# Kernel optimization log

Measured on AMD Instinct MI355X. Metric: run time of the kernel, lower is better.

Reference implementation:

```python
import jax, jax.numpy as jnp
import numpy as np
from jax import lax

V, E, H, K = 100000, 256, 512, 12
B, T = 64, 256
START, END, PAD = 10, 11, 0
NEG = -100000.0


def setup_inputs() -> dict:
    key = jax.random.key(0)
    ks = jax.random.split(key, 16)
    Hd = H // 2
    def n(k, shape, s=0.1):
        return jax.random.normal(k, shape, jnp.float32) * s
    sentence = jax.random.randint(ks[0], (B, T), 0, V)
    sentence_chars = jnp.zeros((B, T, 16), jnp.int32)
    emb = jax.random.normal(ks[1], (V, E), jnp.float32)
    Wih_f, Whh_f = n(ks[2], (4 * Hd, E)), n(ks[3], (4 * Hd, Hd))
    bih_f, bhh_f = n(ks[4], (4 * Hd,)), n(ks[5], (4 * Hd,))
    Wih_b, Whh_b = n(ks[6], (4 * Hd, E)), n(ks[7], (4 * Hd, Hd))
    bih_b, bhh_b = n(ks[8], (4 * Hd,)), n(ks[9], (4 * Hd,))
    Wp, bp = n(ks[10], (K, H)), n(ks[11], (K,))
    # transitions[i, j] = score of transitioning from tag j to tag i
    trans = jax.random.normal(ks[12], (K, K), jnp.float32)
    trans = trans.at[START, :].set(NEG)
    trans = trans.at[:, END].set(NEG)
    trans = trans.at[:, PAD].set(NEG)
    trans = trans.at[PAD, :].set(NEG)
    trans = trans.at[PAD, PAD].set(0.0)
    trans = trans.at[PAD, END].set(0.0)
    h0 = jax.random.normal(ks[13], (2, B, Hd), jnp.float32)
    c0 = jax.random.normal(ks[14], (2, B, Hd), jnp.float32)
    return dict(sentence=sentence, sentence_chars=sentence_chars, emb=emb,
                Wih_f=Wih_f, Whh_f=Whh_f, bih_f=bih_f, bhh_f=bhh_f,
                Wih_b=Wih_b, Whh_b=Whh_b, bih_b=bih_b, bhh_b=bhh_b,
                Wp=Wp, bp=bp, transitions=trans, h0=h0, c0=c0)


def _lstm_dir(x, Wih, Whh, bih, bhh, h, c, reverse):
    # x: [B, T, E] -> hs: [B, T, Hd]; PyTorch LSTM gate order i,f,g,o
    def step(carry, xt):
        h, c = carry
        g = xt @ Wih.T + bih + h @ Whh.T + bhh
        i, f, gg, o = jnp.split(g, 4, axis=-1)
        c = jax.nn.sigmoid(f) * c + jax.nn.sigmoid(i) * jnp.tanh(gg)
        h = jax.nn.sigmoid(o) * jnp.tanh(c)
        return (h, c), h
    _, hs = lax.scan(step, (h, c), jnp.swapaxes(x, 0, 1), reverse=reverse)
    return jnp.swapaxes(hs, 0, 1)


def _viterbi(features, transitions, lengths):
    b, t, k = features.shape
    score0 = jnp.full((b, k), -10000.0, features.dtype).at[:, START].set(0.0)
    def step(score, feat_t):
        m = score[:, None, :] + transitions[None]  # [B, K(to), K(from)]
        bptr = jnp.argmax(m, axis=-1)              # [B, K]
        new = jnp.max(m, axis=-1) + feat_t
        return new, bptr
    final, bptrs = lax.scan(step, score0, jnp.swapaxes(features, 0, 1))  # bptrs [T,B,K]
    best_score = jnp.max(final, axis=-1)
    best_tag = jnp.argmax(final, axis=-1)
    ts = jnp.arange(t)
    def backtrack(x, inp):
        tt, bp = inp  # bp: [B, K]
        emit = x      # p_t (valid where tt < length)
        nxt = jnp.take_along_axis(bp, x[:, None], axis=1)[:, 0]
        x = jnp.where(tt < lengths, nxt, x)
        return x, emit
    _, ps = lax.scan(backtrack, best_tag, (ts, bptrs), reverse=True)  # [T, B]
    paths = jnp.swapaxes(ps, 0, 1)
    paths = jnp.where(jnp.arange(t)[None, :] < lengths[:, None], paths, -1)
    return paths, best_score


def reference(sentence, sentence_chars, emb, Wih_f, Whh_f, bih_f, bhh_f,
              Wih_b, Whh_b, bih_b, bhh_b, Wp, bp, transitions, h0, c0):
    mask = sentence > 0
    lengths = mask.sum(axis=1)
    x = emb[sentence]  # [B, T, E]
    hf = _lstm_dir(x, Wih_f, Whh_f, bih_f, bhh_f, h0[0], c0[0], False)
    hb = _lstm_dir(x, Wih_b, Whh_b, bih_b, bhh_b, h0[1], c0[1], True)
    feats = jnp.concatenate([hf, hb], axis=-1) @ Wp.T + bp  # [B, T, K]
    paths, best_score = _viterbi(feats, transitions, lengths)
    return paths, best_score
```

## Files before the change

### kernel.cpp

```cpp
#include <hip/hip_runtime.h>


#define NB 64
#define NT 256
#define NKTAG 12
#define START_TAG 10
#define KK_SLAB 32
#define KK_REG 16
#define KK_STRM 8

typedef unsigned short u16;
typedef _Float16 half2v __attribute__((ext_vector_type(2)));
typedef _Float16 half8 __attribute__((ext_vector_type(8)));
typedef float f32x4 __attribute__((ext_vector_type(4)));

__device__ __forceinline__ float b2f(u16 u) {
  union { unsigned int i; float f; } v; v.i = ((unsigned int)u) << 16; return v.f;
}
__device__ __forceinline__ u16 f2b(float f) {
  union { float f; unsigned int i; } v; v.f = f;
  unsigned int r = v.i + 0x7FFFu + ((v.i >> 16) & 1u);
  return (u16)(r >> 16);
}
__device__ __forceinline__ u16 f2h(float f) {
  union { _Float16 h; u16 u; } v; v.h = (_Float16)f; return v.u;
}
__device__ __forceinline__ unsigned int pkh(float x, float y) {
  return (unsigned int)f2h(x) | ((unsigned int)f2h(y) << 16);
}
__device__ __forceinline__ float fsig(float x) { return 1.0f / (1.0f + __expf(-x)); }
__device__ __forceinline__ float ftanh(float x) { return 2.0f / (1.0f + __expf(-2.0f * x)) - 1.0f; }

__device__ __forceinline__ float dot2h(unsigned int a, unsigned int b, float c) {
#if __has_builtin(__builtin_amdgcn_fdot2)
  union { unsigned int u; half2v h; } va, vb;
  va.u = a; vb.u = b;
  return __builtin_amdgcn_fdot2(va.h, vb.h, c, false);
#else
  float d;
  asm("v_dot2_f32_f16 %0, %1, %2, %3" : "=v"(d) : "v"(a), "v"(b), "v"(c));
  return d;
#endif
}

__global__ __launch_bounds__(256) void pack_whh(const float* __restrict__ Whf,
                                                const float* __restrict__ Whb,
                                                const float* __restrict__ Wp,
                                                uint4* __restrict__ WT,
                                                unsigned int* __restrict__ WpH) {
  if (blockIdx.x == 256) {
    for (int it = 0; it < 12; ++it) {
      int idx = it * 256 + threadIdx.x;
      int k = idx >> 8, cc = idx & 255;
      WpH[idx] = pkh(Wp[(size_t)k * 512 + 2 * cc], Wp[(size_t)k * 512 + 2 * cc + 1]);
    }
    return;
  }
  int gid = blockIdx.x * 256 + threadIdx.x;
  int d = gid >> 15;
  int rem = gid & 32767;
  int kk = rem >> 8, j = rem & 255;
  const float* W = d ? Whb : Whf;
  int k0 = kk * 2;
  uint4 o;
  o.x = pkh(W[(size_t)j * 256 + k0],         W[(size_t)j * 256 + k0 + 1]);
  o.y = pkh(W[(size_t)(j + 256) * 256 + k0], W[(size_t)(j + 256) * 256 + k0 + 1]);
  o.z = pkh(W[(size_t)(j + 512) * 256 + k0], W[(size_t)(j + 512) * 256 + k0 + 1]);
  o.w = pkh(W[(size_t)(j + 768) * 256 + k0], W[(size_t)(j + 768) * 256 + k0 + 1]);
  WT[gid] = o;
}

__global__ __launch_bounds__(256) void gemm_x(const int* __restrict__ sent,
                                              const float* __restrict__ emb,
                                              const float* __restrict__ Wf,
                                              const float* __restrict__ Wb,
                                              const float* __restrict__ bihf,
                                              const float* __restrict__ bhhf,
                                              const float* __restrict__ bihb,
                                              const float* __restrict__ bhhb,
                                              u16* __restrict__ X4) {
  __shared__ _Float16 A_lds[128][40];
  __shared__ _Float16 B_lds[64][40];
  __shared__ int tok[128];
  __shared__ u16 Xs[128][80];
  int tid = threadIdx.x;
  int lin = blockIdx.y * 32 + blockIdx.x;
  int swz = (lin & 7) * 512 + (lin >> 3);
  int in = swz & 31;
  int im = swz >> 5;
  int d = in >> 4, j0 = (in & 15) * 16;
  if (tid < 128) tok[tid] = sent[im * 128 + tid];

  int w = tid >> 6, l = tid & 63;
  int lrow = l & 15, lk = l >> 4;
  f32x4 acc[2][4];
#pragma unroll
  for (int mt = 0; mt < 2; ++mt)
#pragma unroll
    for (int nt = 0; nt < 4; ++nt) acc[mt][nt] = (f32x4)0.0f;

  int arow = tid >> 1, akh = tid & 1;
  int brow = tid & 63, bkq = tid >> 6;
  int r_w = ((brow >> 4) << 8) + j0 + (brow & 15);
  const float* wrow = (d ? Wb : Wf) + (size_t)r_w * 256;

  for (int kc = 0; kc < 8; ++kc) {
    int k0 = kc * 32;
    __syncthreads();
    {
      const float* ap = emb + (size_t)tok[arow] * 256 + k0 + akh * 16;
#pragma unroll
      for (int q = 0; q < 2; ++q) {
        float4 v0 = *(const float4*)(ap + q * 8);
        float4 v1 = *(const float4*)(ap + q * 8 + 4);
        uint4 pk;
        pk.x = pkh(v0.x, v0.y); pk.y = pkh(v0.z, v0.w);
        pk.z = pkh(v1.x, v1.y); pk.w = pkh(v1.z, v1.w);
        *(uint4*)&A_lds[arow][akh * 16 + q * 8] = pk;
      }
    }
    {
      float4 v0 = *(const float4*)(wrow + k0 + bkq * 8);
      float4 v1 = *(const float4*)(wrow + k0 + bkq * 8 + 4);
      uint4 pk;
      pk.x = pkh(v0.x, v0.y); pk.y = pkh(v0.z, v0.w);
      pk.z = pkh(v1.x, v1.y); pk.w = pkh(v1.z, v1.w);
      *(uint4*)&B_lds[brow][bkq * 8] = pk;
    }
    __syncthreads();
    half8 af[2], bf[4];
#pragma unroll
    for (int mt = 0; mt < 2; ++mt)
      af[mt] = *(const half8*)&A_lds[w * 32 + mt * 16 + lrow][lk * 8];
#pragma unroll
    for (int nt = 0; nt < 4; ++nt)
      bf[nt] = *(const half8*)&B_lds[nt * 16 + lrow][lk * 8];
#pragma unroll
    for (int mt = 0; mt < 2; ++mt)
#pragma unroll
      for (int nt = 0; nt < 4; ++nt)
        acc[mt][nt] = __builtin_amdgcn_mfma_f32_16x16x32_f16(af[mt], bf[nt], acc[mt][nt], 0, 0, 0);
  }
  float bias[4];
#pragma unroll
  for (int nt = 0; nt < 4; ++nt) {
    int rr = nt * 256 + j0 + lrow;
    bias[nt] = d ? (bihb[rr] + bhhb[rr]) : (bihf[rr] + bhhf[rr]);
  }
  __syncthreads();
#pragma unroll
  for (int mt = 0; mt < 2; ++mt)
#pragma unroll
    for (int r = 0; r < 4; ++r) {
      int row = w * 32 + mt * 16 + lk * 4 + r;
      uint2 pk;
      pk.x = (unsigned int)f2b(acc[mt][0][r] + bias[0]) |
             ((unsigned int)f2b(acc[mt][1][r] + bias[1]) << 16);
      pk.y = (unsigned int)f2b(acc[mt][2][r] + bias[2]) |
             ((unsigned int)f2b(acc[mt][3][r] + bias[3]) << 16);
      *(uint2*)&Xs[row][lrow * 4] = pk;
    }
  __syncthreads();
  int frow = tid >> 1, fh = tid & 1;
  int i = im * 128 + frow;
  int bb = i >> 8, tt = i & 255;
  size_t base = (((size_t)d * NT + tt) * NB + bb) * 1024 + (size_t)j0 * 4 + fh * 32;
#pragma unroll
  for (int q = 0; q < 4; ++q)
    *(uint4*)&X4[base + q * 8] = *(const uint4*)&Xs[frow][fh * 32 + q * 8];
}

__global__ __launch_bounds__(1024, 4) void lstm_scan(const uint4* __restrict__ WT,
                                                     const ushort4* __restrict__ X4,
                                                     const float* __restrict__ h0,
                                                     const float* __restrict__ c0,
                                                     u16* __restrict__ H) {
  int d = blockIdx.x >> 6, b = blockIdx.x & 63;
  int tid = threadIdx.x;
  int jj = tid & 255, g = tid >> 8;
  __shared__ uint4 wlds[KK_SLAB * 256];
  __shared__ uint4 h2s4[32];
  __shared__ float4 plds[3][256];
  const uint4* Ws = WT + (size_t)d * 32768;
  for (int e = tid; e < KK_SLAB * 256; e += 1024) wlds[e] = Ws[e];
  uint4 wreg[KK_REG];
#pragma unroll
  for (int r = 0; r < KK_REG; ++r)
    wreg[r] = Ws[(size_t)(KK_SLAB + g * KK_REG + r) * 256 + jj];
  float c = 0.f;
  if (g == 0) c = c0[((size_t)d * NB + b) * 256 + jj];
  if (tid < 256) ((u16*)h2s4)[tid] = f2h(h0[((size_t)d * NB + b) * 256 + tid]);
  __syncthreads();
  for (int s = 0; s < NT; ++s) {
    int t = d ? (NT - 1 - s) : s;
    ushort4 xg = make_ushort4(0, 0, 0, 0);
    if (g == 0) xg = X4[(((size_t)d * NT + t) * NB + b) * 256 + jj];
    float ai = 0.f, af = 0.f, ag = 0.f, ao = 0.f;
    {
      uint4 hc0 = h2s4[24 + g * 2], hc1 = h2s4[24 + g * 2 + 1];
      unsigned int hp[8] = {hc0.x, hc0.y, hc0.z, hc0.w, hc1.x, hc1.y, hc1.z, hc1.w};
      const uint4* Wp_ = Ws + (size_t)(96 + g * 8) * 256 + jj;
#pragma unroll
      for (int u = 0; u < KK_STRM; ++u) {
        uint4 wv = Wp_[(size_t)u * 256];
        ai = dot2h(wv.x, hp[u], ai); af = dot2h(wv.y, hp[u], af);
        ag = dot2h(wv.z, hp[u], ag); ao = dot2h(wv.w, hp[u], ao);
      }
    }
    {
      uint4 ha0 = h2s4[g * 2], ha1 = h2s4[g * 2 + 1];
      unsigned int hp[8] = {ha0.x, ha0.y, ha0.z, ha0.w, ha1.x, ha1.y, ha1.z, ha1.w};
#pragma unroll
      for (int r = 0; r < 8; ++r) {
        uint4 wv = wlds[((g * 8 + r) << 8) | jj];
        ai = dot2h(wv.x, hp[r], ai); af = dot2h(wv.y, hp[r], af);
        ag = dot2h(wv.z, hp[r], ag); ao = dot2h(wv.w, hp[r], ao);
      }
    }
    {
      uint4 hb0 = h2s4[8 + g * 4], hb1 = h2s4[8 + g * 4 + 1];
      uint4 hb2 = h2s4[8 + g * 4 + 2], hb3 = h2s4[8 + g * 4 + 3];
      unsigned int hp[16] = {hb0.x, hb0.y, hb0.z, hb0.w, hb1.x, hb1.y, hb1.z, hb1.w,
                             hb2.x, hb2.y, hb2.z, hb2.w, hb3.x, hb3.y, hb3.z, hb3.w};
#pragma unroll
      for (int r = 0; r < KK_REG; ++r) {
        uint4 wv = wreg[r];
        ai = dot2h(wv.x, hp[r], ai); af = dot2h(wv.y, hp[r], af);
        ag = dot2h(wv.z, hp[r], ag); ao = dot2h(wv.w, hp[r], ao);
      }
    }
    if (g) plds[g - 1][jj] = make_float4(ai, af, ag, ao);
    __syncthreads();
    if (g == 0) {
      float4 p0 = plds[0][jj], p1 = plds[1][jj], p2 = plds[2][jj];
      ai += p0.x + p1.x + p2.x + b2f(xg.x);
      af += p0.y + p1.y + p2.y + b2f(xg.y);
      ag += p0.z + p1.z + p2.z + b2f(xg.z);
      ao += p0.w + p1.w + p2.w + b2f(xg.w);
      float ii = fsig(ai), ff = fsig(af), gg = ftanh(ag), oo = fsig(ao);
      c = ff * c + ii * gg;
      float h = oo * ftanh(c);
      u16 hu = f2h(h);
      ((u16*)h2s4)[jj] = hu;
      H[(((size_t)d * NB + b) * NT + t) * 256 + jj] = hu;
    }
    __syncthreads();
  }
}

__global__ __launch_bounds__(384) void feats_kernel(const u16* __restrict__ H,
                                                    const unsigned int* __restrict__ WpH,
                                                    const float* __restrict__ bp,
                                                    float* __restrict__ FT) {
  __shared__ uint4 hbuf[32][65];
  __shared__ uint4 wbuf[64][12];
  int tid = threadIdx.x;
  int i0 = blockIdx.x * 32;
  for (int idx = tid; idx < 768; idx += 384) {
    int it = idx / 12, k = idx - it * 12;
    wbuf[it][k] = ((const uint4*)WpH)[k * 64 + it];
  }
  for (int idx = tid; idx < 2048; idx += 384) {
    int row = idx >> 6, c4 = idx & 63;
    int i = i0 + row;
    int b = i >> 8, t = i & 255;
    int dd = c4 >> 5, cc = c4 & 31;
    const uint4* hpg = (const uint4*)(H + (((size_t)dd * NB + b) * NT + t) * 256);
    hbuf[row][c4] = hpg[cc];
  }
  __syncthreads();
  int row = tid / 12, k = tid - row * 12;
  float s0 = 0.f, s1 = 0.f, s2 = 0.f, s3 = 0.f;
#pragma unroll 8
  for (int it = 0; it < 64; ++it) {
    uint4 h4 = hbuf[row][it];
    uint4 w4 = wbuf[it][k];
    s0 = dot2h(h4.x, w4.x, s0); s1 = dot2h(h4.y, w4.y, s1);
    s2 = dot2h(h4.z, w4.z, s2); s3 = dot2h(h4.w, w4.w, s3);
  }
  int i = i0 + row;
  FT[(size_t)i * NKTAG + k] = (s0 + s1) + (s2 + s3) + bp[k];
}

__global__ __launch_bounds__(64) void viterbi_kernel(const float* __restrict__ FT,
                                                     const float* __restrict__ trans,
                                                     const int* __restrict__ sent,
                                                     float* __restrict__ out) {
  int b = blockIdx.x, tid = threadIdx.x;
  __shared__ float trans_s[12][12];
  __shared__ float s_s[12];
  __shared__ unsigned char bp_s[256][12];
  __shared__ int path_s[256];
  for (int idx = tid; idx < 144; idx += 64) trans_s[idx / 12][idx % 12] = trans[idx];
  int cnt = 0;
#pragma unroll
  for (int q = 0; q < 4; ++q) cnt += (sent[b * NT + q * 64 + tid] > 0) ? 1 : 0;
  for (int off = 32; off; off >>= 1) cnt += __shfl_down(cnt, off);
  int len = __shfl(cnt, 0);
  if (tid < 12) s_s[tid] = (tid == START_TAG) ? 0.f : -10000.f;
  float f_next = (tid < 12) ? FT[((size_t)b * NT) * NKTAG + tid] : 0.f;
  __syncthreads();
  for (int t = 0; t < NT; ++t) {
    float best = 0.f, f = f_next;
    int barg = 0;
    if (t + 1 < NT && tid < 12)
      f_next = FT[((size_t)b * NT + t + 1) * NKTAG + tid];
    if (tid < 12) {
      best = s_s[0] + trans_s[tid][0];
      barg = 0;
#pragma unroll
      for (int fr = 1; fr < 12; ++fr) {
        float v = s_s[fr] + trans_s[tid][fr];
        if (v > best) { best = v; barg = fr; }
      }
    }
    __syncthreads();
    if (tid < 12) {
      s_s[tid] = best + f;
      bp_s[t][tid] = (unsigned char)barg;
    }
    __syncthreads();
  }
  if (tid == 0) {
    float bs = s_s[0];
    int bt = 0;
    for (int k = 1; k < 12; ++k)
      if (s_s[k] > bs) { bs = s_s[k]; bt = k; }
    out[NB * NT + b] = bs;
    int x = bt;
    for (int tt = NT - 1; tt >= 0; --tt) {
      path_s[tt] = x;
      int nxt = bp_s[tt][x];
      if (tt < len) x = nxt;
    }
  }
  __syncthreads();
#pragma unroll
  for (int q = 0; q < 4; ++q) {
    int t = q * 64 + tid;
    out[b * NT + t] = (t < len) ? (float)path_s[t] : -1.0f;
  }
}

extern "C" void kernel_launch(void* const* d_in, const int* in_sizes, int n_in,
                              void* d_out, int out_size, void* d_ws, size_t ws_size,
                              hipStream_t stream) {
  (void)in_sizes; (void)n_in; (void)out_size; (void)ws_size;
  const int*   sent  = (const int*)d_in[0];
  const float* emb   = (const float*)d_in[2];
  const float* Wih_f = (const float*)d_in[3];
  const float* Whh_f = (const float*)d_in[4];
  const float* bih_f = (const float*)d_in[5];
  const float* bhh_f = (const float*)d_in[6];
  const float* Wih_b = (const float*)d_in[7];
  const float* Whh_b = (const float*)d_in[8];
  const float* bih_b = (const float*)d_in[9];
  const float* bhh_b = (const float*)d_in[10];
  const float* Wp    = (const float*)d_in[11];
  const float* bp    = (const float*)d_in[12];
  const float* trans = (const float*)d_in[13];
  const float* h0    = (const float*)d_in[14];
  const float* c0    = (const float*)d_in[15];
  float* out = (float*)d_out;

  char* w = (char*)d_ws;
  u16*   X4  = (u16*)w;
  uint4* WTH = (uint4*)(w + 67108864);
  float* FT  = (float*)(w + 68157440);
  unsigned int* WpH = (unsigned int*)(w + 68943872);
  u16*   H   = (u16*)(w + 68956160);

  pack_whh<<<dim3(257), dim3(256), 0, stream>>>(Whh_f, Whh_b, Wp, WTH, WpH);
  gemm_x<<<dim3(32, 128), dim3(256), 0, stream>>>(sent, emb, Wih_f, Wih_b,
                                                  bih_f, bhh_f, bih_b, bhh_b, X4);
  lstm_scan<<<dim3(128), dim3(1024), 0, stream>>>(WTH, (const ushort4*)X4, h0, c0, H);
  feats_kernel<<<dim3(512), dim3(384), 0, stream>>>(H, WpH, bp, FT);
  viterbi_kernel<<<dim3(64), dim3(64), 0, stream>>>(FT, trans, sent, out);
}
```

Measured before the change: 602.0 us.

## Split LSTM recurrence over 512 threads with more weights held in registers

The recurrent scan now uses 2 thread groups of 256 instead of 4, so each thread covers 64 of the 128 packed hidden pairs. Of those 64 weight rows, 46 are kept in registers and 18 in LDS, and the per-step global weight streaming is removed. This halves the partial-sum reduction through LDS and drops global loads from the serial loop. In exchange, register pressure per thread rises sharply (46 uint4), which risks spills, and each thread's dot-product chain is longer.

```diff
diff --git a/kernel.cpp b/kernel.cpp
--- a/kernel.cpp
+++ b/kernel.cpp
@@ -5,9 +5,8 @@
 #define NT 256
 #define NKTAG 12
 #define START_TAG 10
-#define KK_SLAB 32
-#define KK_REG 16
-#define KK_STRM 8
+#define KK_SLAB2 18
+#define KK_REG2 46
 
 typedef unsigned short u16;
 typedef _Float16 half2v __attribute__((ext_vector_type(2)));
@@ -170,23 +169,27 @@
     *(uint4*)&X4[base + q * 8] = *(const uint4*)&Xs[frow][fh * 32 + q * 8];
 }
 
-__global__ __launch_bounds__(1024, 4) void lstm_scan(const uint4* __restrict__ WT,
-                                                     const ushort4* __restrict__ X4,
-                                                     const float* __restrict__ h0,
-                                                     const float* __restrict__ c0,
-                                                     u16* __restrict__ H) {
+__global__ __launch_bounds__(512, 2) void lstm_scan(const uint4* __restrict__ WT,
+                                                    const ushort4* __restrict__ X4,
+                                                    const float* __restrict__ h0,
+                                                    const float* __restrict__ c0,
+                                                    u16* __restrict__ H) {
   int d = blockIdx.x >> 6, b = blockIdx.x & 63;
   int tid = threadIdx.x;
   int jj = tid & 255, g = tid >> 8;
-  __shared__ uint4 wlds[KK_SLAB * 256];
+  __shared__ uint4 wlds[2 * KK_SLAB2 * 256];
   __shared__ uint4 h2s4[32];
-  __shared__ float4 plds[3][256];
+  __shared__ float4 plds[256];
   const uint4* Ws = WT + (size_t)d * 32768;
-  for (int e = tid; e < KK_SLAB * 256; e += 1024) wlds[e] = Ws[e];
-  uint4 wreg[KK_REG];
-#pragma unroll
-  for (int r = 0; r < KK_REG; ++r)
-    wreg[r] = Ws[(size_t)(KK_SLAB + g * KK_REG + r) * 256 + jj];
+  for (int e = tid; e < 2 * KK_SLAB2 * 256; e += 512) {
+    int sr = e >> 8, j2 = e & 255;
+    int gg = sr / KK_SLAB2, r = sr - gg * KK_SLAB2;
+    wlds[e] = Ws[(size_t)(gg * 64 + r) * 256 + j2];
+  }
+  uint4 wreg[KK_REG2];
+#pragma unroll
+  for (int r = 0; r < KK_REG2; ++r)
+    wreg[r] = Ws[(size_t)(g * 64 + KK_SLAB2 + r) * 256 + jj];
   float c = 0.f;
   if (g == 0) c = c0[((size_t)d * NB + b) * 256 + jj];
   if (tid < 256) ((u16*)h2s4)[tid] = f2h(h0[((size_t)d * NB + b) * 256 + tid]);
@@ -196,49 +199,30 @@
     ushort4 xg = make_ushort4(0, 0, 0, 0);
     if (g == 0) xg = X4[(((size_t)d * NT + t) * NB + b) * 256 + jj];
     float ai = 0.f, af = 0.f, ag = 0.f, ao = 0.f;
-    {
-      uint4 hc0 = h2s4[24 + g * 2], hc1 = h2s4[24 + g * 2 + 1];
-      unsigned int hp[8] = {hc0.x, hc0.y, hc0.z, hc0.w, hc1.x, hc1.y, hc1.z, hc1.w};
-      const uint4* Wp_ = Ws + (size_t)(96 + g * 8) * 256 + jj;
-#pragma unroll
-      for (int u = 0; u < KK_STRM; ++u) {
-        uint4 wv = Wp_[(size_t)u * 256];
-        ai = dot2h(wv.x, hp[u], ai); af = dot2h(wv.y, hp[u], af);
-        ag = dot2h(wv.z, hp[u], ag); ao = dot2h(wv.w, hp[u], ao);
+#pragma unroll
+    for (int q = 0; q < 16; ++q) {
+      uint4 h4 = h2s4[g * 16 + q];
+      unsigned int hp[4] = {h4.x, h4.y, h4.z, h4.w};
+#pragma unroll
+      for (int e = 0; e < 4; ++e) {
+        int kkl = q * 4 + e;
+        uint4 wv;
+        if (kkl < KK_SLAB2) wv = wlds[((g * KK_SLAB2 + kkl) << 8) | jj];
+        else                wv = wreg[kkl - KK_SLAB2];
+        ai = dot2h(wv.x, hp[e], ai); af = dot2h(wv.y, hp[e], af);
+        ag = dot2h(wv.z, hp[e], ag); ao = dot2h(wv.w, hp[e], ao);
       }
     }
-    {
-      uint4 ha0 = h2s4[g * 2], ha1 = h2s4[g * 2 + 1];
-      unsigned int hp[8] = {ha0.x, ha0.y, ha0.z, ha0.w, ha1.x, ha1.y, ha1.z, ha1.w};
-#pragma unroll
-      for (int r = 0; r < 8; ++r) {
-        uint4 wv = wlds[((g * 8 + r) << 8) | jj];
-        ai = dot2h(wv.x, hp[r], ai); af = dot2h(wv.y, hp[r], af);
-        ag = dot2h(wv.z, hp[r], ag); ao = dot2h(wv.w, hp[r], ao);
-      }
-    }
-    {
-      uint4 hb0 = h2s4[8 + g * 4], hb1 = h2s4[8 + g * 4 + 1];
-      uint4 hb2 = h2s4[8 + g * 4 + 2], hb3 = h2s4[8 + g * 4 + 3];
-      unsigned int hp[16] = {hb0.x, hb0.y, hb0.z, hb0.w, hb1.x, hb1.y, hb1.z, hb1.w,
-                             hb2.x, hb2.y, hb2.z, hb2.w, hb3.x, hb3.y, hb3.z, hb3.w};
-#pragma unroll
-      for (int r = 0; r < KK_REG; ++r) {
-        uint4 wv = wreg[r];
-        ai = dot2h(wv.x, hp[r], ai); af = dot2h(wv.y, hp[r], af);
-        ag = dot2h(wv.z, hp[r], ag); ao = dot2h(wv.w, hp[r], ao);
-      }
-    }
-    if (g) plds[g - 1][jj] = make_float4(ai, af, ag, ao);
+    if (g) plds[jj] = make_float4(ai, af, ag, ao);
     __syncthreads();
     if (g == 0) {
-      float4 p0 = plds[0][jj], p1 = plds[1][jj], p2 = plds[2][jj];
-      ai += p0.x + p1.x + p2.x + b2f(xg.x);
-      af += p0.y + p1.y + p2.y + b2f(xg.y);
-      ag += p0.z + p1.z + p2.z + b2f(xg.z);
-      ao += p0.w + p1.w + p2.w + b2f(xg.w);
-      float ii = fsig(ai), ff = fsig(af), gg = ftanh(ag), oo = fsig(ao);
-      c = ff * c + ii * gg;
+      float4 p0 = plds[jj];
+      ai += p0.x + b2f(xg.x);
+      af += p0.y + b2f(xg.y);
+      ag += p0.z + b2f(xg.z);
+      ao += p0.w + b2f(xg.w);
+      float ii = fsig(ai), ff = fsig(af), gg2 = ftanh(ag), oo = fsig(ao);
+      c = ff * c + ii * gg2;
       float h = oo * ftanh(c);
       u16 hu = f2h(h);
       ((u16*)h2s4)[jj] = hu;
@@ -373,7 +357,7 @@
   pack_whh<<<dim3(257), dim3(256), 0, stream>>>(Whh_f, Whh_b, Wp, WTH, WpH);
   gemm_x<<<dim3(32, 128), dim3(256), 0, stream>>>(sent, emb, Wih_f, Wih_b,
                                                   bih_f, bhh_f, bih_b, bhh_b, X4);
-  lstm_scan<<<dim3(128), dim3(1024), 0, stream>>>(WTH, (const ushort4*)X4, h0, c0, H);
+  lstm_scan<<<dim3(128), dim3(512), 0, stream>>>(WTH, (const ushort4*)X4, h0, c0, H);
   feats_kernel<<<dim3(512), dim3(384), 0, stream>>>(H, WpH, bp, FT);
   viterbi_kernel<<<dim3(64), dim3(64), 0, stream>>>(FT, trans, sent, out);
 }
```

Measured after the change: 566.5 us. 5.9% less time.
